# Performance work log

Measured on AMD Instinct MI355X. Metric: run time of the kernel, lower is better.

## Reference

```python
import jax, jax.numpy as jnp
import numpy as np


def setup_inputs() -> dict:
    key = jax.random.key(0)
    k1, k2 = jax.random.split(key)
    B, T, D, K = 256, 196, 768, 4
    z = jax.random.normal(k1, (B, T, D), dtype=jnp.float32)
    gt_dT = jax.random.normal(k2, (B, T, T, K), dtype=jnp.float32)
    sigma = jnp.ones((K,), dtype=jnp.float32)
    return {"z": z, "gt_dT": gt_dT, "sigma": sigma}


def reference(z, gt_dT, sigma):
    B, T, D = z.shape
    # Gaussian (RBF) kernel over pairwise patch-transform deltas: [B,T,T]
    kernel = jnp.sum(gt_dT * gt_dT / (2.0 * sigma * sigma), axis=-1)
    w = jnp.exp(-kernel)                                   # [B,T,T]
    z2 = jnp.sum(z * z, axis=-1)                           # [B,T]
    w_col_sum = jnp.sum(w, axis=2)                         # [B,T]
    term1 = jnp.sum(z2 * w_col_sum, axis=1)                # [B]
    wz = jnp.einsum('btu,bud->btd', w, z)                  # [B,T,D]
    term2 = jnp.sum(wz * z, axis=(1, 2))                   # [B]
    w_row_sum = jnp.sum(w, axis=1)                         # [B,T]
    term3 = jnp.sum(z2 * w_row_sum, axis=1)                # [B]
    loss = jnp.mean(term1 - 2.0 * term2 + term3) / (T * T)
    return loss
```

## Files before the change

### kernel.cpp

```cpp
#include <hip/hip_runtime.h>
#include <hip/hip_bf16.h>


typedef __attribute__((ext_vector_type(8))) __bf16 bf16x8;
typedef __attribute__((ext_vector_type(4))) float f32x4;

#define NB   256
#define TT   196
#define DD   768
#define TTT  (TT * TT)
#define BK   32
#define NKS  (DD / BK)
#define ZPAD 40


#define ATH 512

__device__ __forceinline__ bf16x8 pack8(const float4& a, const float4& b) {
    bf16x8 v;
    v[0] = (__bf16)a.x; v[1] = (__bf16)a.y; v[2] = (__bf16)a.z; v[3] = (__bf16)a.w;
    v[4] = (__bf16)b.x; v[5] = (__bf16)b.y; v[6] = (__bf16)b.z; v[7] = (__bf16)b.w;
    return v;
}
__device__ __forceinline__ float sq8(const float4& a, const float4& b) {
    return a.x*a.x + a.y*a.y + a.z*a.z + a.w*a.w
         + b.x*b.x + b.y*b.y + b.z*b.z + b.w*b.w;
}

__global__ __launch_bounds__(ATH)
void gram_kernel(const float* __restrict__ z,
                 float* __restrict__ G,
                 float* __restrict__ z2g)
{
    __shared__ __bf16 Zt[2][208][ZPAD];

    const int hw = blockIdx.x;
    const int lb = (hw & 7) * 64 + (hw >> 3);
    const int b  = lb >> 1;
    const int s  = lb & 1;

    const int tid  = threadIdx.x;
    const int lane = tid & 63;
    const int wid  = tid >> 6;

    const int  srow = tid >> 2;
    const int  scol = (tid & 3) << 3;
    const int  row1 = srow + 128;
    const bool r1st = row1 < 208;
    const bool r1v  = row1 < TT;
    const float* zp0 = z + ((size_t)b * TT + srow) * DD + scol;
    const float* zp1 = z + ((size_t)b * TT + row1) * DD + scol;

    f32x4 acc[13];
#pragma unroll
    for (int j = 0; j < 13; ++j) acc[j] = (f32x4){0.f, 0.f, 0.f, 0.f};

    float z2p0 = 0.f, z2p1 = 0.f;

    {
        float4 a0 = *(const float4*)(zp0);
        float4 a1 = *(const float4*)(zp0 + 4);
        z2p0 += sq8(a0, a1);
        *(bf16x8*)&Zt[0][srow][scol] = pack8(a0, a1);
        if (r1st) {
            float4 b0 = make_float4(0.f,0.f,0.f,0.f), b1 = make_float4(0.f,0.f,0.f,0.f);
            if (r1v) { b0 = *(const float4*)(zp1); b1 = *(const float4*)(zp1 + 4); }
            z2p1 += sq8(b0, b1);
            *(bf16x8*)&Zt[0][row1][scol] = pack8(b0, b1);
        }
    }

    int arow = s * 128 + (wid << 4) + (lane & 15);
    if (arow > 207) arow = 207;
    const int koff = (lane >> 4) << 3;

    int cur = 0;
#pragma unroll 1
    for (int ks = 0; ks < NKS; ++ks) {
        __syncthreads();
        const bool more = (ks + 1) < NKS;

        float4 a0, a1, b0, b1;
        a0 = a1 = b0 = b1 = make_float4(0.f,0.f,0.f,0.f);
        if (more) {
            const float* p0 = zp0 + (ks + 1) * BK;
            a0 = *(const float4*)(p0);
            a1 = *(const float4*)(p0 + 4);
            if (r1v) {
                const float* p1 = zp1 + (ks + 1) * BK;
                b0 = *(const float4*)(p1);
                b1 = *(const float4*)(p1 + 4);
            }
        }

        bf16x8 af = *(const bf16x8*)&Zt[cur][arow][koff];
#pragma unroll
        for (int j = 0; j < 13; ++j) {
            bf16x8 bfr = *(const bf16x8*)&Zt[cur][(j << 4) + (lane & 15)][koff];
            acc[j] = __builtin_amdgcn_mfma_f32_16x16x32_bf16(af, bfr, acc[j], 0, 0, 0);
        }

        if (more) {
            z2p0 += sq8(a0, a1);
            *(bf16x8*)&Zt[cur ^ 1][srow][scol] = pack8(a0, a1);
            if (r1st) {
                z2p1 += sq8(b0, b1);
                *(bf16x8*)&Zt[cur ^ 1][row1][scol] = pack8(b0, b1);
            }
        }
        cur ^= 1;
    }

    float zz0 = z2p0 + __shfl_xor(z2p0, 1); zz0 += __shfl_xor(zz0, 2);
    float zz1 = z2p1 + __shfl_xor(z2p1, 1); zz1 += __shfl_xor(zz1, 2);
    if (s == 0 && (tid & 3) == 0) {
        z2g[b * TT + srow] = zz0;
        if (r1v) z2g[b * TT + row1] = zz1;
    }

    const int l15 = lane & 15;
    const int lq  = lane >> 4;
#pragma unroll
    for (int j = 0; j < 13; ++j) {
        const int u = (j << 4) + l15;
        if (u >= TT) continue;
#pragma unroll
        for (int r = 0; r < 4; ++r) {
            const int t = s * 128 + (wid << 4) + (lq << 2) + r;
            if (t < TT) G[((size_t)b * TT + t) * TT + u] = acc[j][r];
        }
    }
}


#define BTH   256
#define BGRID 2048

__global__ __launch_bounds__(BTH)
void loss_kernel(const float4* __restrict__ gt4,
                 const float* __restrict__ G,
                 const float* __restrict__ z2g,
                 const float* __restrict__ sigma,
                 float* __restrict__ partials)
{
    const int tid = threadIdx.x;
    const float4 sg = *(const float4*)sigma;
    const float c0 = 0.5f / (sg.x * sg.x);
    const float c1 = 0.5f / (sg.y * sg.y);
    const float c2 = 0.5f / (sg.z * sg.z);
    const float c3 = 0.5f / (sg.w * sg.w);

    const unsigned total  = NB * TTT;
    const unsigned stride = BTH * BGRID;
    float lsum = 0.f;

    for (unsigned q = blockIdx.x * BTH + tid; q < total; q += stride) {
        const unsigned b  = q / TTT;
        const unsigned rr = q - b * TTT;
        const unsigned t  = rr / TT;
        const unsigned u  = rr - t * TT;

        const float4 g   = gt4[q];
        const float  Gtu = G[q];
        const float  z2t = z2g[b * TT + t];
        const float  z2u = z2g[b * TT + u];

        const float sS = g.x*g.x*c0 + g.y*g.y*c1 + g.z*g.z*c2 + g.w*g.w*c3;
        lsum += __expf(-sS) * (z2t + z2u - 2.f * Gtu);
    }

#pragma unroll
    for (int off = 32; off > 0; off >>= 1) lsum += __shfl_xor(lsum, off);

    __shared__ float red[BTH / 64];
    if ((tid & 63) == 0) red[tid >> 6] = lsum;
    __syncthreads();
    if (tid == 0) {
        float s = 0.f;
#pragma unroll
        for (int w = 0; w < BTH / 64; ++w) s += red[w];
        partials[blockIdx.x] = s;
    }
}


__global__ __launch_bounds__(256)
void finalize_kernel(const float* __restrict__ partials, float* __restrict__ out)
{
    const int tid = threadIdx.x;
    float s = 0.f;
#pragma unroll
    for (int k = 0; k < BGRID / 256; ++k) s += partials[tid + k * 256];
#pragma unroll
    for (int off = 32; off > 0; off >>= 1) s += __shfl_xor(s, off);
    __shared__ float red[4];
    if ((tid & 63) == 0) red[tid >> 6] = s;
    __syncthreads();
    if (tid == 0) {
        float tot = red[0] + red[1] + red[2] + red[3];
        out[0] = tot * (1.0f / ((float)NB * (float)TT * (float)TT));
    }
}


#define TP  208
#define NW  13
#define NTH (NW * 64)

__global__ __launch_bounds__(NTH)
void patch_loss_fused(const float* __restrict__ z,
                      const float* __restrict__ gt,
                      const float* __restrict__ sigma,
                      float* __restrict__ out)
{
    __shared__ __bf16 Zt[2][TP][BK];
    __shared__ float z2s[TP];
    __shared__ float red[NW];

    const int b    = blockIdx.x;
    const int tid  = threadIdx.x;
    const int lane = tid & 63;
    const int wid  = tid >> 6;

    const int  srow = tid >> 2;
    const int  scol = (tid & 3) << 3;
    const bool srv  = srow < TT;
    const float* zrow = z + ((size_t)b * TT + srow) * DD + scol;

    f32x4 acc[NW];
#pragma unroll
    for (int j = 0; j < NW; ++j) acc[j] = (f32x4){0.f, 0.f, 0.f, 0.f};
    float z2p = 0.f;
    {
        float4 r0 = make_float4(0.f,0.f,0.f,0.f), r1 = make_float4(0.f,0.f,0.f,0.f);
        if (srv) { r0 = *(const float4*)(zrow); r1 = *(const float4*)(zrow + 4); }
        z2p += sq8(r0, r1);
        *(bf16x8*)&Zt[0][srow][scol] = pack8(r0, r1);
    }
    const int arow = (wid << 4) + (lane & 15);
    const int koff = (lane >> 4) << 3;
    int cur = 0;
#pragma unroll 1
    for (int ks = 0; ks < NKS; ++ks) {
        __syncthreads();
        const bool more = (ks + 1) < NKS;
        float4 r0 = make_float4(0.f,0.f,0.f,0.f), r1 = make_float4(0.f,0.f,0.f,0.f);
        if (more && srv) {
            const float* p = zrow + (ks + 1) * BK;
            r0 = *(const float4*)(p); r1 = *(const float4*)(p + 4);
        }
        bf16x8 af = *(const bf16x8*)&Zt[cur][arow][koff];
#pragma unroll
        for (int j = 0; j < NW; ++j) {
            bf16x8 bfr = *(const bf16x8*)&Zt[cur][(j << 4) + (lane & 15)][koff];
            acc[j] = __builtin_amdgcn_mfma_f32_16x16x32_bf16(af, bfr, acc[j], 0, 0, 0);
        }
        if (more) {
            z2p += sq8(r0, r1);
            *(bf16x8*)&Zt[cur ^ 1][srow][scol] = pack8(r0, r1);
        }
        cur ^= 1;
    }
    float zz = z2p + __shfl_xor(z2p, 1);
    zz += __shfl_xor(zz, 2);
    if ((tid & 3) == 0) z2s[srow] = srv ? zz : 0.f;
    __syncthreads();

    const float4 sg = *(const float4*)sigma;
    const float c0 = 0.5f / (sg.x * sg.x);
    const float c1 = 0.5f / (sg.y * sg.y);
    const float c2 = 0.5f / (sg.z * sg.z);
    const float c3 = 0.5f / (sg.w * sg.w);
    const int l15 = lane & 15;
    const int lq  = lane >> 4;
    int   trow[4]; float z2t[4]; size_t tbase[4];
#pragma unroll
    for (int r = 0; r < 4; ++r) {
        const int t = (wid << 4) + (lq << 2) + r;
        trow[r] = t; z2t[r] = z2s[t];
        tbase[r] = ((size_t)b * TT + t) * TT;
    }
    const float4* gtp = (const float4*)gt;
    float lsum = 0.f;
#pragma unroll
    for (int j = 0; j < NW; ++j) {
        const int  u  = (j << 4) + l15;
        const bool uv = u < TT;
        const float z2u = z2s[u];
        float4 dv[4];
#pragma unroll
        for (int r = 0; r < 4; ++r) {
            const bool v = uv && (trow[r] < TT);
            dv[r] = v ? gtp[tbase[r] + u] : make_float4(0.f,0.f,0.f,0.f);
        }
#pragma unroll
        for (int r = 0; r < 4; ++r) {
            const bool v = uv && (trow[r] < TT);
            if (v) {
                const float sS = dv[r].x*dv[r].x*c0 + dv[r].y*dv[r].y*c1
                               + dv[r].z*dv[r].z*c2 + dv[r].w*dv[r].w*c3;
                lsum += __expf(-sS) * (z2t[r] + z2u - 2.f * acc[j][r]);
            }
        }
    }
#pragma unroll
    for (int off = 32; off > 0; off >>= 1) lsum += __shfl_xor(lsum, off);
    if (lane == 0) red[wid] = lsum;
    __syncthreads();
    if (tid == 0) {
        float sum = 0.f;
#pragma unroll
        for (int w = 0; w < NW; ++w) sum += red[w];
        atomicAdd(out, sum * (1.0f / ((float)NB * (float)TT * (float)TT)));
    }
}


extern "C" void kernel_launch(void* const* d_in, const int* in_sizes, int n_in,
                              void* d_out, int out_size, void* d_ws, size_t ws_size,
                              hipStream_t stream) {
    const float* z     = (const float*)d_in[0];
    const float* gt    = (const float*)d_in[1];
    const float* sigma = (const float*)d_in[2];
    float* out = (float*)d_out;

    const size_t G_elems  = (size_t)NB * TTT;
    const size_t z2_elems = (size_t)NB * TT;
    const size_t need = (G_elems + z2_elems + BGRID) * sizeof(float);

    if (ws_size >= need) {
        float* G        = (float*)d_ws;
        float* z2g      = G + G_elems;
        float* partials = z2g + z2_elems;

        gram_kernel<<<dim3(512), dim3(ATH), 0, stream>>>(z, G, z2g);
        loss_kernel<<<dim3(BGRID), dim3(BTH), 0, stream>>>(
            (const float4*)gt, G, z2g, sigma, partials);
        finalize_kernel<<<dim3(1), dim3(256), 0, stream>>>(partials, out);
    } else {
        hipMemsetAsync(out, 0, sizeof(float), stream);
        patch_loss_fused<<<dim3(NB), dim3(NTH), 0, stream>>>(z, gt, sigma, out);
    }
}
```

Before: 330.0 us.

## Widen Gram K-slab to 64, balance row split, unroll loss loop by four

The Gram kernel now stages 64-wide K slabs instead of 32, which halves the number of barriers, and splits the 196 rows 112/84 across the two blocks per batch so fewer warps idle on padding rows. The loss kernel batches four strided iterations so more global loads are in flight at once, and both kernels get occupancy launch bounds. The fallback fused kernel is reworked to the same two-block split. The cost is more LDS per block and more registers, which could lower occupancy.

```diff
diff --git a/kernel.cpp b/kernel.cpp
--- a/kernel.cpp
+++ b/kernel.cpp
@@ -9,12 +9,9 @@
 #define TT   196
 #define DD   768
 #define TTT  (TT * TT)
-#define BK   32
-#define NKS  (DD / BK)
-#define ZPAD 40
-
-
-#define ATH 512
+#define BK2  64
+#define NSLAB (DD / BK2)
+#define ZPAD 72
 
 __device__ __forceinline__ bf16x8 pack8(const float4& a, const float4& b) {
     bf16x8 v;
@@ -27,10 +24,11 @@
          + b.x*b.x + b.y*b.y + b.z*b.z + b.w*b.w;
 }
 
-__global__ __launch_bounds__(ATH)
-void gram_kernel(const float* __restrict__ z,
-                 float* __restrict__ G,
-                 float* __restrict__ z2g)
+
+__global__ __launch_bounds__(512, 4)
+void gram_k(const float* __restrict__ z,
+            float* __restrict__ G,
+            float* __restrict__ z2g)
 {
     __shared__ __bf16 Zt[2][208][ZPAD];
 
@@ -38,6 +36,222 @@
     const int lb = (hw & 7) * 64 + (hw >> 3);
     const int b  = lb >> 1;
     const int s  = lb & 1;
+    const int nmf = 7 - s;
+
+    const int tid  = threadIdx.x;
+    const int lane = tid & 63;
+    const int wid  = tid >> 6;
+
+    const int r0   = tid >> 3;
+    const int scol = (tid & 7) << 3;
+    const bool seg3 = (r0 < 16);
+    const int rows[4] = { r0, r0 + 64, r0 + 128, r0 + 192 };
+    const float* zb = z + (size_t)b * TT * DD + scol;
+
+    f32x4 acc[13];
+#pragma unroll
+    for (int j = 0; j < 13; ++j) acc[j] = (f32x4){0.f, 0.f, 0.f, 0.f};
+    float z2p[4] = {0.f, 0.f, 0.f, 0.f};
+
+#pragma unroll
+    for (int g = 0; g < 4; ++g) {
+        if (g == 3 && !seg3) continue;
+        const int  row = rows[g];
+        const bool v   = row < TT;
+        float4 a0 = make_float4(0.f,0.f,0.f,0.f), a1 = a0;
+        if (v) {
+            const float* p = zb + (size_t)row * DD;
+            a0 = *(const float4*)(p);
+            a1 = *(const float4*)(p + 4);
+        }
+        z2p[g] += sq8(a0, a1);
+        *(bf16x8*)&Zt[0][row][scol] = pack8(a0, a1);
+    }
+
+    const int arow = (s * 112 + (wid << 4) + (lane & 15)) % 208;
+    const int koff = (lane >> 4) << 3;
+
+    int cur = 0;
+#pragma unroll 1
+    for (int ks = 0; ks < NSLAB; ++ks) {
+        __syncthreads();
+        const bool more = (ks + 1) < NSLAB;
+
+        float4 L0[4], L1[4];
+#pragma unroll
+        for (int g = 0; g < 4; ++g) {
+            L0[g] = make_float4(0.f,0.f,0.f,0.f); L1[g] = L0[g];
+            if (more && !(g == 3 && !seg3) && rows[g] < TT) {
+                const float* p = zb + (size_t)rows[g] * DD + (ks + 1) * BK2;
+                L0[g] = *(const float4*)(p);
+                L1[g] = *(const float4*)(p + 4);
+            }
+        }
+
+        if (wid < nmf) {
+            bf16x8 af0 = *(const bf16x8*)&Zt[cur][arow][koff];
+            bf16x8 af1 = *(const bf16x8*)&Zt[cur][arow][32 + koff];
+#pragma unroll
+            for (int j = 0; j < 13; ++j) {
+                bf16x8 b0 = *(const bf16x8*)&Zt[cur][(j << 4) + (lane & 15)][koff];
+                acc[j] = __builtin_amdgcn_mfma_f32_16x16x32_bf16(af0, b0, acc[j], 0, 0, 0);
+            }
+#pragma unroll
+            for (int j = 0; j < 13; ++j) {
+                bf16x8 b1 = *(const bf16x8*)&Zt[cur][(j << 4) + (lane & 15)][32 + koff];
+                acc[j] = __builtin_amdgcn_mfma_f32_16x16x32_bf16(af1, b1, acc[j], 0, 0, 0);
+            }
+        }
+
+        if (more) {
+#pragma unroll
+            for (int g = 0; g < 4; ++g) {
+                if (g == 3 && !seg3) continue;
+                z2p[g] += sq8(L0[g], L1[g]);
+                *(bf16x8*)&Zt[cur ^ 1][rows[g]][scol] = pack8(L0[g], L1[g]);
+            }
+        }
+        cur ^= 1;
+    }
+
+    if (s == 0) {
+#pragma unroll
+        for (int g = 0; g < 4; ++g) {
+            if (g == 3 && !seg3) continue;
+            float v = z2p[g];
+            v += __shfl_xor(v, 1); v += __shfl_xor(v, 2); v += __shfl_xor(v, 4);
+            if ((tid & 7) == 0 && rows[g] < TT) z2g[b * TT + rows[g]] = v;
+        }
+    }
+
+    if (wid < nmf) {
+        const int l15 = lane & 15;
+        const int lq  = lane >> 4;
+#pragma unroll
+        for (int j = 0; j < 13; ++j) {
+            const int u = (j << 4) + l15;
+            if (u >= TT) continue;
+#pragma unroll
+            for (int r = 0; r < 4; ++r) {
+                const int t = s * 112 + (wid << 4) + (lq << 2) + r;
+                if (t < TT) G[((size_t)b * TT + t) * TT + u] = acc[j][r];
+            }
+        }
+    }
+}
+
+
+#define BTH   256
+#define BGRID 2048
+
+__global__ __launch_bounds__(BTH, 8)
+void loss_k(const float4* __restrict__ gt4,
+            const float* __restrict__ G,
+            const float* __restrict__ z2g,
+            const float* __restrict__ sigma,
+            float* __restrict__ partials)
+{
+    const int tid = threadIdx.x;
+    const float4 sg = *(const float4*)sigma;
+    const float c0 = 0.5f / (sg.x * sg.x);
+    const float c1 = 0.5f / (sg.y * sg.y);
+    const float c2 = 0.5f / (sg.z * sg.z);
+    const float c3 = 0.5f / (sg.w * sg.w);
+
+    const unsigned total = NB * TTT;
+    const unsigned S     = BTH * BGRID;
+    unsigned q = blockIdx.x * BTH + tid;
+    float lsum = 0.f;
+
+#pragma unroll 1
+    while (q + 3 * S < total) {
+        unsigned qs[4];
+        float4 g[4]; float Gv[4], zt[4], zu[4];
+#pragma unroll
+        for (int k = 0; k < 4; ++k) qs[k] = q + k * S;
+#pragma unroll
+        for (int k = 0; k < 4; ++k) {
+            const unsigned b  = qs[k] / TTT;
+            const unsigned rr = qs[k] - b * TTT;
+            const unsigned t  = rr / TT;
+            const unsigned u  = rr - t * TT;
+            g[k]  = gt4[qs[k]];
+            Gv[k] = G[qs[k]];
+            zt[k] = z2g[b * TT + t];
+            zu[k] = z2g[b * TT + u];
+        }
+#pragma unroll
+        for (int k = 0; k < 4; ++k) {
+            const float sS = g[k].x*g[k].x*c0 + g[k].y*g[k].y*c1
+                           + g[k].z*g[k].z*c2 + g[k].w*g[k].w*c3;
+            lsum += __expf(-sS) * (zt[k] + zu[k] - 2.f * Gv[k]);
+        }
+        q += 4 * S;
+    }
+#pragma unroll 1
+    while (q < total) {
+        const unsigned b  = q / TTT;
+        const unsigned rr = q - b * TTT;
+        const unsigned t  = rr / TT;
+        const unsigned u  = rr - t * TT;
+        const float4 g = gt4[q];
+        const float sS = g.x*g.x*c0 + g.y*g.y*c1 + g.z*g.z*c2 + g.w*g.w*c3;
+        lsum += __expf(-sS) * (z2g[b * TT + t] + z2g[b * TT + u] - 2.f * G[q]);
+        q += S;
+    }
+
+#pragma unroll
+    for (int off = 32; off > 0; off >>= 1) lsum += __shfl_xor(lsum, off);
+    __shared__ float red[BTH / 64];
+    if ((tid & 63) == 0) red[tid >> 6] = lsum;
+    __syncthreads();
+    if (tid == 0) {
+        float t = 0.f;
+#pragma unroll
+        for (int w = 0; w < BTH / 64; ++w) t += red[w];
+        partials[blockIdx.x] = t;
+    }
+}
+
+
+__global__ __launch_bounds__(256)
+void final_k(const float* __restrict__ partials, float* __restrict__ out)
+{
+    const int tid = threadIdx.x;
+    float s = 0.f;
+#pragma unroll
+    for (int k = 0; k < BGRID / 256; ++k) s += partials[tid + k * 256];
+#pragma unroll
+    for (int off = 32; off > 0; off >>= 1) s += __shfl_xor(s, off);
+    __shared__ float red[4];
+    if ((tid & 63) == 0) red[tid >> 6] = s;
+    __syncthreads();
+    if (tid == 0)
+        out[0] = (red[0] + red[1] + red[2] + red[3])
+               * (1.0f / ((float)NB * (float)TT * (float)TT));
+}
+
+
+#define BK 32
+#define NKS (DD / BK)
+#define ZP2 40
+#define NTH 512
+
+__global__ __launch_bounds__(NTH)
+void patch_loss_fused2(const float* __restrict__ z,
+                       const float* __restrict__ gt,
+                       const float* __restrict__ sigma,
+                       float* __restrict__ out)
+{
+    __shared__ __bf16 Zt[2][208][ZP2];
+    __shared__ float z2s[208];
+    __shared__ float red[8];
+
+    const int hw = blockIdx.x;
+    const int lb = (hw & 7) * 64 + (hw >> 3);
+    const int b  = lb >> 1;
+    const int s  = lb & 1;
+    const int nmf = 7 - s;
 
     const int tid  = threadIdx.x;
     const int lane = tid & 63;
@@ -54,52 +268,44 @@
     f32x4 acc[13];
 #pragma unroll
     for (int j = 0; j < 13; ++j) acc[j] = (f32x4){0.f, 0.f, 0.f, 0.f};
-
     float z2p0 = 0.f, z2p1 = 0.f;
-
     {
         float4 a0 = *(const float4*)(zp0);
         float4 a1 = *(const float4*)(zp0 + 4);
         z2p0 += sq8(a0, a1);
         *(bf16x8*)&Zt[0][srow][scol] = pack8(a0, a1);
         if (r1st) {
-            float4 b0 = make_float4(0.f,0.f,0.f,0.f), b1 = make_float4(0.f,0.f,0.f,0.f);
+            float4 b0 = make_float4(0.f,0.f,0.f,0.f), b1 = b0;
             if (r1v) { b0 = *(const float4*)(zp1); b1 = *(const float4*)(zp1 + 4); }
             z2p1 += sq8(b0, b1);
             *(bf16x8*)&Zt[0][row1][scol] = pack8(b0, b1);
         }
     }
-
-    int arow = s * 128 + (wid << 4) + (lane & 15);
-    if (arow > 207) arow = 207;
+    const int arow = s * 112 + (wid << 4) + (lane & 15);
     const int koff = (lane >> 4) << 3;
-
     int cur = 0;
 #pragma unroll 1
     for (int ks = 0; ks < NKS; ++ks) {
         __syncthreads();
         const bool more = (ks + 1) < NKS;
-
         float4 a0, a1, b0, b1;
         a0 = a1 = b0 = b1 = make_float4(0.f,0.f,0.f,0.f);
         if (more) {
             const float* p0 = zp0 + (ks + 1) * BK;
-            a0 = *(const float4*)(p0);
-            a1 = *(const float4*)(p0 + 4);
+            a0 = *(const float4*)(p0); a1 = *(const float4*)(p0 + 4);
             if (r1v) {
                 const float* p1 = zp1 + (ks + 1) * BK;
-                b0 = *(const float4*)(p1);
-                b1 = *(const float4*)(p1 + 4);
-            }
-        }
-
-        bf16x8 af = *(const bf16x8*)&Zt[cur][arow][koff];
-#pragma unroll
-        for (int j = 0; j < 13; ++j) {
-            bf16x8 bfr = *(const bf16x8*)&Zt[cur][(j << 4) + (lane & 15)][koff];
-            acc[j] = __builtin_amdgcn_mfma_f32_16x16x32_bf16(af, bfr, acc[j], 0, 0, 0);
-        }
-
+                b0 = *(const float4*)(p1); b1 = *(const float4*)(p1 + 4);
+            }
+        }
+        if (wid < nmf) {
+            bf16x8 af = *(const bf16x8*)&Zt[cur][arow][koff];
+#pragma unroll
+            for (int j = 0; j < 13; ++j) {
+                bf16x8 bfr = *(const bf16x8*)&Zt[cur][(j << 4) + (lane & 15)][koff];
+                acc[j] = __builtin_amdgcn_mfma_f32_16x16x32_bf16(af, bfr, acc[j], 0, 0, 0);
+            }
+        }
         if (more) {
             z2p0 += sq8(a0, a1);
             *(bf16x8*)&Zt[cur ^ 1][srow][scol] = pack8(a0, a1);
@@ -110,160 +316,12 @@
         }
         cur ^= 1;
     }
-
     float zz0 = z2p0 + __shfl_xor(z2p0, 1); zz0 += __shfl_xor(zz0, 2);
     float zz1 = z2p1 + __shfl_xor(z2p1, 1); zz1 += __shfl_xor(zz1, 2);
-    if (s == 0 && (tid & 3) == 0) {
-        z2g[b * TT + srow] = zz0;
-        if (r1v) z2g[b * TT + row1] = zz1;
-    }
-
-    const int l15 = lane & 15;
-    const int lq  = lane >> 4;
-#pragma unroll
-    for (int j = 0; j < 13; ++j) {
-        const int u = (j << 4) + l15;
-        if (u >= TT) continue;
-#pragma unroll
-        for (int r = 0; r < 4; ++r) {
-            const int t = s * 128 + (wid << 4) + (lq << 2) + r;
-            if (t < TT) G[((size_t)b * TT + t) * TT + u] = acc[j][r];
-        }
-    }
-}
-
-
-#define BTH   256
-#define BGRID 2048
-
-__global__ __launch_bounds__(BTH)
-void loss_kernel(const float4* __restrict__ gt4,
-                 const float* __restrict__ G,
-                 const float* __restrict__ z2g,
-                 const float* __restrict__ sigma,
-                 float* __restrict__ partials)
-{
-    const int tid = threadIdx.x;
-    const float4 sg = *(const float4*)sigma;
-    const float c0 = 0.5f / (sg.x * sg.x);
-    const float c1 = 0.5f / (sg.y * sg.y);
-    const float c2 = 0.5f / (sg.z * sg.z);
-    const float c3 = 0.5f / (sg.w * sg.w);
-
-    const unsigned total  = NB * TTT;
-    const unsigned stride = BTH * BGRID;
-    float lsum = 0.f;
-
-    for (unsigned q = blockIdx.x * BTH + tid; q < total; q += stride) {
-        const unsigned b  = q / TTT;
-        const unsigned rr = q - b * TTT;
-        const unsigned t  = rr / TT;
-        const unsigned u  = rr - t * TT;
-
-        const float4 g   = gt4[q];
-        const float  Gtu = G[q];
-        const float  z2t = z2g[b * TT + t];
-        const float  z2u = z2g[b * TT + u];
-
-        const float sS = g.x*g.x*c0 + g.y*g.y*c1 + g.z*g.z*c2 + g.w*g.w*c3;
-        lsum += __expf(-sS) * (z2t + z2u - 2.f * Gtu);
-    }
-
-#pragma unroll
-    for (int off = 32; off > 0; off >>= 1) lsum += __shfl_xor(lsum, off);
-
-    __shared__ float red[BTH / 64];
-    if ((tid & 63) == 0) red[tid >> 6] = lsum;
-    __syncthreads();
-    if (tid == 0) {
-        float s = 0.f;
-#pragma unroll
-        for (int w = 0; w < BTH / 64; ++w) s += red[w];
-        partials[blockIdx.x] = s;
-    }
-}
-
-
-__global__ __launch_bounds__(256)
-void finalize_kernel(const float* __restrict__ partials, float* __restrict__ out)
-{
-    const int tid = threadIdx.x;
-    float s = 0.f;
-#pragma unroll
-    for (int k = 0; k < BGRID / 256; ++k) s += partials[tid + k * 256];
-#pragma unroll
-    for (int off = 32; off > 0; off >>= 1) s += __shfl_xor(s, off);
-    __shared__ float red[4];
-    if ((tid & 63) == 0) red[tid >> 6] = s;
-    __syncthreads();
-    if (tid == 0) {
-        float tot = red[0] + red[1] + red[2] + red[3];
-        out[0] = tot * (1.0f / ((float)NB * (float)TT * (float)TT));
-    }
-}
-
-
-#define TP  208
-#define NW  13
-#define NTH (NW * 64)
-
-__global__ __launch_bounds__(NTH)
-void patch_loss_fused(const float* __restrict__ z,
-                      const float* __restrict__ gt,
-                      const float* __restrict__ sigma,
-                      float* __restrict__ out)
-{
-    __shared__ __bf16 Zt[2][TP][BK];
-    __shared__ float z2s[TP];
-    __shared__ float red[NW];
-
-    const int b    = blockIdx.x;
-    const int tid  = threadIdx.x;
-    const int lane = tid & 63;
-    const int wid  = tid >> 6;
-
-    const int  srow = tid >> 2;
-    const int  scol = (tid & 3) << 3;
-    const bool srv  = srow < TT;
-    const float* zrow = z + ((size_t)b * TT + srow) * DD + scol;
-
-    f32x4 acc[NW];
-#pragma unroll
-    for (int j = 0; j < NW; ++j) acc[j] = (f32x4){0.f, 0.f, 0.f, 0.f};
-    float z2p = 0.f;
-    {
-        float4 r0 = make_float4(0.f,0.f,0.f,0.f), r1 = make_float4(0.f,0.f,0.f,0.f);
-        if (srv) { r0 = *(const float4*)(zrow); r1 = *(const float4*)(zrow + 4); }
-        z2p += sq8(r0, r1);
-        *(bf16x8*)&Zt[0][srow][scol] = pack8(r0, r1);
-    }
-    const int arow = (wid << 4) + (lane & 15);
-    const int koff = (lane >> 4) << 3;
-    int cur = 0;
-#pragma unroll 1
-    for (int ks = 0; ks < NKS; ++ks) {
-        __syncthreads();
-        const bool more = (ks + 1) < NKS;
-        float4 r0 = make_float4(0.f,0.f,0.f,0.f), r1 = make_float4(0.f,0.f,0.f,0.f);
-        if (more && srv) {
-            const float* p = zrow + (ks + 1) * BK;
-            r0 = *(const float4*)(p); r1 = *(const float4*)(p + 4);
-        }
-        bf16x8 af = *(const bf16x8*)&Zt[cur][arow][koff];
-#pragma unroll
-        for (int j = 0; j < NW; ++j) {
-            bf16x8 bfr = *(const bf16x8*)&Zt[cur][(j << 4) + (lane & 15)][koff];
-            acc[j] = __builtin_amdgcn_mfma_f32_16x16x32_bf16(af, bfr, acc[j], 0, 0, 0);
-        }
-        if (more) {
-            z2p += sq8(r0, r1);
-            *(bf16x8*)&Zt[cur ^ 1][srow][scol] = pack8(r0, r1);
-        }
-        cur ^= 1;
-    }
-    float zz = z2p + __shfl_xor(z2p, 1);
-    zz += __shfl_xor(zz, 2);
-    if ((tid & 3) == 0) z2s[srow] = srv ? zz : 0.f;
+    if ((tid & 3) == 0) {
+        z2s[srow] = zz0;
+        if (r1st) z2s[row1] = r1v ? zz1 : 0.f;
+    }
     __syncthreads();
 
     const float4 sg = *(const float4*)sigma;
@@ -273,33 +331,36 @@
     const float c3 = 0.5f / (sg.w * sg.w);
     const int l15 = lane & 15;
     const int lq  = lane >> 4;
-    int   trow[4]; float z2t[4]; size_t tbase[4];
-#pragma unroll
-    for (int r = 0; r < 4; ++r) {
-        const int t = (wid << 4) + (lq << 2) + r;
-        trow[r] = t; z2t[r] = z2s[t];
-        tbase[r] = ((size_t)b * TT + t) * TT;
-    }
-    const float4* gtp = (const float4*)gt;
     float lsum = 0.f;
-#pragma unroll
-    for (int j = 0; j < NW; ++j) {
-        const int  u  = (j << 4) + l15;
-        const bool uv = u < TT;
-        const float z2u = z2s[u];
-        float4 dv[4];
+    if (wid < nmf) {
+        int trow[4]; float z2t[4]; size_t tbase[4];
 #pragma unroll
         for (int r = 0; r < 4; ++r) {
-            const bool v = uv && (trow[r] < TT);
-            dv[r] = v ? gtp[tbase[r] + u] : make_float4(0.f,0.f,0.f,0.f);
-        }
-#pragma unroll
-        for (int r = 0; r < 4; ++r) {
-            const bool v = uv && (trow[r] < TT);
-            if (v) {
-                const float sS = dv[r].x*dv[r].x*c0 + dv[r].y*dv[r].y*c1
-                               + dv[r].z*dv[r].z*c2 + dv[r].w*dv[r].w*c3;
-                lsum += __expf(-sS) * (z2t[r] + z2u - 2.f * acc[j][r]);
+            const int t = s * 112 + (wid << 4) + (lq << 2) + r;
+            trow[r] = t;
+            z2t[r]  = (t < TT) ? z2s[t] : 0.f;
+            tbase[r] = ((size_t)b * TT + (t < TT ? t : 0)) * TT;
+        }
+        const float4* gtp = (const float4*)gt;
+#pragma unroll
+        for (int j = 0; j < 13; ++j) {
+            const int  u  = (j << 4) + l15;
+            const bool uv = u < TT;
+            const float z2u = uv ? z2s[u] : 0.f;
+            float4 dv[4];
+#pragma unroll
+            for (int r = 0; r < 4; ++r) {
+                const bool v = uv && (trow[r] < TT);
+                dv[r] = v ? gtp[tbase[r] + u] : make_float4(0.f,0.f,0.f,0.f);
+            }
+#pragma unroll
+            for (int r = 0; r < 4; ++r) {
+                const bool v = uv && (trow[r] < TT);
+                if (v) {
+                    const float sS = dv[r].x*dv[r].x*c0 + dv[r].y*dv[r].y*c1
+                                   + dv[r].z*dv[r].z*c2 + dv[r].w*dv[r].w*c3;
+                    lsum += __expf(-sS) * (z2t[r] + z2u - 2.f * acc[j][r]);
+                }
             }
         }
     }
@@ -308,10 +369,10 @@
     if (lane == 0) red[wid] = lsum;
     __syncthreads();
     if (tid == 0) {
-        float sum = 0.f;
-#pragma unroll
-        for (int w = 0; w < NW; ++w) sum += red[w];
-        atomicAdd(out, sum * (1.0f / ((float)NB * (float)TT * (float)TT)));
+        float t = 0.f;
+#pragma unroll
+        for (int w = 0; w < 8; ++w) t += red[w];
+        atomicAdd(out, t * (1.0f / ((float)NB * (float)TT * (float)TT)));
     }
 }
 
@@ -332,13 +393,12 @@
         float* G        = (float*)d_ws;
         float* z2g      = G + G_elems;
         float* partials = z2g + z2_elems;
-
-        gram_kernel<<<dim3(512), dim3(ATH), 0, stream>>>(z, G, z2g);
-        loss_kernel<<<dim3(BGRID), dim3(BTH), 0, stream>>>(
+        gram_k <<<dim3(512),  dim3(512), 0, stream>>>(z, G, z2g);
+        loss_k <<<dim3(BGRID), dim3(BTH), 0, stream>>>(
             (const float4*)gt, G, z2g, sigma, partials);
-        finalize_kernel<<<dim3(1), dim3(256), 0, stream>>>(partials, out);
+        final_k<<<dim3(1),    dim3(256), 0, stream>>>(partials, out);
     } else {
         hipMemsetAsync(out, 0, sizeof(float), stream);
-        patch_loss_fused<<<dim3(NB), dim3(NTH), 0, stream>>>(z, gt, sigma, out);
-    }
-}
+        patch_loss_fused2<<<dim3(512), dim3(NTH), 0, stream>>>(z, gt, sigma, out);
+    }
+}
```

After: 333.9 us. About the same (+1.2%).
